# Performance work log

Hardware: AMD Instinct MI355X
Metric: run time of the kernel (lower is better)

## Reference

```python
import jax, jax.numpy as jnp
import numpy as np

B, C, V, L = 64, 32, 1024, 12
C_OUT = 64
ORDER = 2
C_CAT = (ORDER * 3 + 1) * C  # 224


def setup_inputs() -> dict:
    key = jax.random.key(0)
    ks = jax.random.split(key, 6)
    x = jax.random.normal(ks[0], (B, C, V, L), dtype=jnp.float32)
    # random non-negative adjacencies, row-normalized like diffusion supports
    def adj(k):
        a = jax.random.uniform(k, (V, V), dtype=jnp.float32)
        return a / jnp.sum(a, axis=1, keepdims=True)
    a0, a1, a2 = adj(ks[1]), adj(ks[2]), adj(ks[3])
    W = jax.random.normal(ks[4], (C_OUT, C_CAT), dtype=jnp.float32) * 0.05
    b = jax.random.normal(ks[5], (C_OUT,), dtype=jnp.float32) * 0.05
    return {"x": x, "a0": a0, "a1": a1, "a2": a2, "W": W, "b": b}


def reference(x, a0, a1, a2, W, b):
    # diffusion propagation: x[b,c,v,l] @ A[v,w] -> [b,c,w,l]
    def prop(z, A):
        return jnp.einsum('ncvl,vw->ncwl', z, A)

    out = [x]
    for A in (a0, a1, a2):
        x1 = prop(x, A)
        out.append(x1)
        x2 = prop(x1, A)  # order=2
        out.append(x2)
    h = jnp.concatenate(out, axis=1)  # [B, 7*C, V, L]
    # 1x1 conv == channel GEMM; dropout is identity at inference
    return jnp.einsum('ncvl,oc->novl', h, W) + b[None, :, None, None]
```

## Files before the change

### kernel.cpp

```cpp
#include <hip/hip_runtime.h>
#include <hip/hip_bf16.h>


typedef __attribute__((ext_vector_type(4))) float  f32x4;
typedef __attribute__((ext_vector_type(8))) short  s16x8;
typedef __attribute__((ext_vector_type(4))) short  s16x4;

__device__ inline short f2bf(float f) {
    unsigned u = __builtin_bit_cast(unsigned, f);
    unsigned r = (u + 0x7FFFu + ((u >> 16) & 1u)) >> 16;
    return (short)r;
}

__device__ inline f32x4 mfma16(s16x8 a, s16x8 b, f32x4 c) {
    return __builtin_amdgcn_mfma_f32_16x16x32_bf16(a, b, c, 0, 0, 0);
}

__device__ inline void gll16(const void* g, void* l) {
    __builtin_amdgcn_global_load_lds(
        (const __attribute__((address_space(1))) void*)g,
        (__attribute__((address_space(3))) void*)l, 16, 0, 0);
}

#define SB0   __builtin_amdgcn_sched_barrier(0)
#define BARM  asm volatile("s_barrier" ::: "memory")
#define LGKM0 asm volatile("s_waitcnt lgkmcnt(0)" ::: "memory")

__global__ __launch_bounds__(256) void cast_x_v2(const float* __restrict__ x,
                                                 short* __restrict__ Xg) {
    __shared__ short Xl[12 * 1040];
    const int bc = blockIdx.x;
    const int t  = threadIdx.x;
    const int b  = bc >> 5;
    const int c  = bc & 31;
    const float4* src = (const float4*)(x + (size_t)bc * 12288);
#pragma unroll
    for (int k = 0; k < 12; ++k) {
        int f4 = k * 256 + t;
        float4 v = src[f4];
        int f  = f4 * 4;
        int vi = f / 12;
        int li = f - vi * 12;
        float vals[4] = {v.x, v.y, v.z, v.w};
#pragma unroll
        for (int e = 0; e < 4; ++e) {
            Xl[li * 1040 + vi] = f2bf(vals[e]);
            if (++li == 12) { li = 0; ++vi; }
        }
    }
    __syncthreads();
#pragma unroll
    for (int k = 0; k < 6; ++k) {
        int ch = k * 256 + t;
        int l  = ch >> 7;
        int v8 = ch & 127;
        *(s16x8*)(Xg + (size_t)(b * 384 + l * 32 + c) * 1024 + v8 * 8) =
            *(const s16x8*)&Xl[l * 1040 + v8 * 8];
    }
}

__global__ __launch_bounds__(256) void cast_a_v2(const float* __restrict__ a0,
                                                 const float* __restrict__ a1,
                                                 const float* __restrict__ a2,
                                                 short* __restrict__ Btall,
                                                 short* __restrict__ Ab) {
    __shared__ float tbuf[32][33];
    const int z = blockIdx.z;
    const float* A = (z == 0) ? a0 : ((z == 1) ? a1 : a2);
    const int v0 = blockIdx.x * 32;
    const int w0 = blockIdx.y * 32;
    const int tr = threadIdx.x >> 3;
    const int tc = (threadIdx.x & 7) << 2;
    float4 val = *(const float4*)&A[(size_t)(v0 + tr) * 1024 + w0 + tc];
    s16x4 sb;
    sb[0] = f2bf(val.x); sb[1] = f2bf(val.y); sb[2] = f2bf(val.z); sb[3] = f2bf(val.w);
    *(s16x4*)(Ab + (size_t)z * 1048576 + (size_t)(v0 + tr) * 1024 + w0 + tc) = sb;
    tbuf[tr][tc + 0] = val.x; tbuf[tr][tc + 1] = val.y;
    tbuf[tr][tc + 2] = val.z; tbuf[tr][tc + 3] = val.w;
    __syncthreads();
    s16x4 st;
#pragma unroll
    for (int i = 0; i < 4; ++i) st[i] = f2bf(tbuf[tc + i][tr]);
    *(s16x4*)(Btall + (size_t)(2 * z) * 1048576 + (size_t)(w0 + tr) * 1024 + v0 + tc) = st;
}

__global__ __launch_bounds__(256, 2) void gemm_bt(const short* __restrict__ Xb, long xz,
                                                  const short* __restrict__ Btb, long bz,
                                                  short* __restrict__ Cb, long cz,
                                                  int crow) {
    __shared__ __align__(16) short Alds[128 * 32];
    __shared__ __align__(16) short Blds[128 * 32];

    const int tid  = threadIdx.x;
    const int lane = tid & 63;
    const int wid  = tid >> 6;
    const int wm   = wid >> 1;
    const int wn   = wid & 1;
    const int m0   = blockIdx.y * 128;
    const int n0   = blockIdx.x * 128;

    const short* X  = Xb  + (size_t)blockIdx.z * xz;
    const short* Bt = Btb + (size_t)blockIdx.z * bz;
    short*       C  = Cb  + (size_t)blockIdx.z * cz;

    const short* Ag = X  + (size_t)(m0 + wid * 32 + (lane >> 2)) * 1024 + (lane & 3) * 8;
    const short* Bg = Bt + (size_t)(n0 + wid * 32 + (lane >> 2)) * 1024 + (lane & 3) * 8;
    short* la = &Alds[wid * 1024];
    short* lb = &Blds[wid * 1024];

    const int lane15 = lane & 15;
    const int lq     = lane >> 4;
    const int ar     = lane15 * 32 + lq * 8;

    f32x4 acc[4][4] = {};

    for (int k0 = 0; k0 < 1024; k0 += 32) {
        __syncthreads();
        gll16(Ag + k0, la);
        gll16(Ag + k0 + 16 * 1024, la + 512);
        gll16(Bg + k0, lb);
        gll16(Bg + k0 + 16 * 1024, lb + 512);
        __syncthreads();

        s16x8 af[4], bf[4];
#pragma unroll
        for (int i = 0; i < 4; ++i)
            af[i] = *(const s16x8*)&Alds[(wm * 64 + i * 16) * 32 + ar];
#pragma unroll
        for (int j = 0; j < 4; ++j)
            bf[j] = *(const s16x8*)&Blds[(wn * 64 + j * 16) * 32 + ar];
#pragma unroll
        for (int i = 0; i < 4; ++i)
#pragma unroll
            for (int j = 0; j < 4; ++j)
                acc[i][j] = mfma16(af[i], bf[j], acc[i][j]);
    }

#pragma unroll
    for (int i = 0; i < 4; ++i) {
        int rbase = m0 + wm * 64 + i * 16 + lq * 4;
#pragma unroll
        for (int r = 0; r < 4; ++r) {
            size_t rowoff = (size_t)(rbase + r) * crow;
#pragma unroll
            for (int j = 0; j < 4; ++j) {
                int col = n0 + wn * 64 + j * 16 + lane15;
                C[rowoff + col] = f2bf(acc[i][j][r]);
            }
        }
    }
}


#define STAGE_A(d, h, kt) do {                                               \
    const short* _s = Agp + (h) * 65536 + (kt) * 64;                         \
    short* _l = lA + (((d) * 2 + (h)) << 13);                                \
    gll16(_s, _l);                                                           \
    gll16(_s + 131072, _l + 4096);                                           \
} while (0)

#define STAGE_B(d, h, kt) do {                                               \
    const short* _s = Bgp + (h) * 32768 + (kt) * 64;                         \
    short* _l = lB + (((d) * 2 + (h)) << 13);                                \
    gll16(_s, _l);                                                           \
    gll16(_s + 131072, _l + 4096);                                           \
} while (0)

#define RD_A(D, MH) do {                                                     \
    const short* _p = Als + (((D) * 2 + (MH)) << 13) + aBase;                \
    _Pragma("unroll")                                                        \
    for (int _fm = 0; _fm < 4; ++_fm) {                                      \
        af[_fm][0] = *(const s16x8*)(_p + _fm * 1024 + slot0);               \
        af[_fm][1] = *(const s16x8*)(_p + _fm * 1024 + (slot0 ^ 32));        \
    }                                                                        \
} while (0)

#define RD_B(D, NH, dst) do {                                                \
    const short* _p = Bls + (((D) * 2 + (NH)) << 13) + bBase;                \
    _Pragma("unroll")                                                        \
    for (int _fn = 0; _fn < 2; ++_fn) {                                      \
        dst[_fn][0] = *(const s16x8*)(_p + _fn * 1024 + slot0);              \
        dst[_fn][1] = *(const s16x8*)(_p + _fn * 1024 + (slot0 ^ 32));       \
    }                                                                        \
} while (0)

#define MM(MH, NH, bv) do {                                                  \
    __builtin_amdgcn_s_setprio(1);                                           \
    _Pragma("unroll")                                                        \
    for (int _fm = 0; _fm < 4; ++_fm) {                                      \
        _Pragma("unroll")                                                    \
        for (int _fn = 0; _fn < 2; ++_fn) {                                  \
            _Pragma("unroll")                                                \
            for (int _kk = 0; _kk < 2; ++_kk)                                \
                acc[(MH) * 4 + _fm][(NH) * 2 + _fn] =                        \
                    mfma16(af[_fm][_kk], bv[_fn][_kk],                       \
                           acc[(MH) * 4 + _fm][(NH) * 2 + _fn]);             \
        }                                                                    \
    }                                                                        \
    __builtin_amdgcn_s_setprio(0);                                           \
} while (0)

#define VM4 asm volatile("s_waitcnt vmcnt(4)" ::: "memory")
#define VM0 asm volatile("s_waitcnt vmcnt(0)" ::: "memory")

#define TILE(D, T, S1, S2, VMST) do {                                        \
                                                             \
    RD_A(D, 0); RD_B(D, 0, bv0);                                             \
    if (S1) STAGE_A(1 - (D), 1, (T) + 1);                                    \
    SB0; BARM; SB0; LGKM0; SB0;                                              \
    MM(0, 0, bv0);                                                           \
    SB0; BARM; SB0;                                                          \
                                                             \
    RD_B(D, 1, bv1);                                                         \
    if (S1) STAGE_B(1 - (D), 1, (T) + 1);                                    \
    SB0; BARM; SB0; LGKM0; SB0;                                              \
    MM(0, 1, bv1);                                                           \
    SB0; BARM; SB0;                                                          \
                                                             \
    RD_A(D, 1);                                                              \
    if (S2) STAGE_A((D), 0, (T) + 2);                                        \
    SB0; BARM; SB0; LGKM0; SB0;                                              \
    MM(1, 1, bv1);                                                           \
    SB0; BARM; SB0;                                                          \
                                                             \
    if (S2) STAGE_B((D), 0, (T) + 2);                                        \
    SB0; BARM; SB0;                                                          \
    MM(1, 0, bv0);                                                           \
    SB0; VMST; BARM; SB0;                                                    \
} while (0)

__global__ __launch_bounds__(512, 2) void gemm256(const short* __restrict__ X,
                                                  const short* __restrict__ Bt,
                                                  short* __restrict__ C) {
    __shared__ __align__(16) short Als[32768];
    __shared__ __align__(16) short Bls[32768];

    const int t    = threadIdx.x;
    const int lane = t & 63;
    const int w    = t >> 6;
    const int wm   = w >> 2;
    const int wn   = w & 3;
    const int r15  = lane & 15;
    const int q    = lane >> 4;
    const int m0   = blockIdx.y << 8;
    const int n0   = blockIdx.x << 8;

    const int srow = t >> 3;
    const int kc8  = (((t & 7) - srow) & 7) * 8;
    const short* Agp = X + (size_t)(m0 + srow) * 1024 + kc8;
    const int rB0  = ((srow >> 5) << 6) | (srow & 31);
    const short* Bgp = Bt + (size_t)(n0 + rB0) * 1024 + kc8;
    short* lA = Als + t * 8;
    short* lB = Bls + t * 8;

    const int slot0 = ((q + r15) & 7) * 8;
    const int aBase = (wm * 64 + r15) * 64;
    const int bBase = (wn * 32 + r15) * 64;

    f32x4 acc[8][4] = {};
    s16x8 af[4][2], bv0[2][2], bv1[2][2];

    STAGE_A(0, 0, 0); STAGE_A(0, 1, 0); STAGE_B(0, 0, 0); STAGE_B(0, 1, 0);
    STAGE_A(1, 0, 1); STAGE_B(1, 0, 1);
    VM4;
    BARM; SB0;

#pragma unroll 1
    for (int it = 0; it < 7; ++it) {
        const int T = it * 2;
        TILE(0, T,     true, true, VM4);
        TILE(1, T + 1, true, true, VM4);
    }
    TILE(0, 14, true,  false, VM0);
    TILE(1, 15, false, false, (void)0);

    const int s_idx  = n0 >> 10;
    const int v_base = (n0 & 1023) + wn * 64 + r15;
    const int ks0    = s_idx * 32 + q * 4;
#pragma unroll
    for (int fmt = 0; fmt < 8; ++fmt) {
        const int gidx = (m0 >> 5) + wm * 4 + (fmt >> 1);
        const int bb   = gidx / 12;
        const int ll   = gidx - bb * 12;
        const int ks   = ks0 + (fmt & 1) * 16;
        const size_t base = (size_t)bb * 12288 + ll;
#pragma unroll
        for (int fnt = 0; fnt < 4; ++fnt) {
            const int v = v_base + fnt * 16;
            s16x4 sv;
            sv[0] = f2bf(acc[fmt][fnt][0]);
            sv[1] = f2bf(acc[fmt][fnt][1]);
            sv[2] = f2bf(acc[fmt][fnt][2]);
            sv[3] = f2bf(acc[fmt][fnt][3]);
            *(s16x4*)(C + (base + (size_t)v * 12) * 192 + ks) = sv;
        }
    }
}

__global__ __launch_bounds__(256, 2) void gemm_fin(const float* __restrict__ x,
                                                   const short* __restrict__ Hc,
                                                   const float* __restrict__ W,
                                                   const float* __restrict__ bias,
                                                   float* __restrict__ out) {
    __shared__ __align__(16) short Wl[64 * 232];
    __shared__ __align__(16) short Hl[3][8192];

    const int t    = threadIdx.x;
    const int lane = t & 63;
    const int wv   = t >> 6;
    const int r15  = lane & 15;
    const int lq   = lane >> 4;
    const int blk  = blockIdx.x;
    const int b    = blk / 48;
    const int p0   = (blk - b * 48) * 256;
    const size_t R0 = (size_t)b * 12288 + p0;

    {
        const int o  = t >> 2;
        const int c0 = (t & 3) * 56;
        const float* wp = W + o * 224 + c0;
        short* d = &Wl[o * 232 + c0];
#pragma unroll
        for (int i = 0; i < 14; ++i) {
            float4 w4 = *(const float4*)(wp + i * 4);
            s16x4 s;
            s[0] = f2bf(w4.x); s[1] = f2bf(w4.y); s[2] = f2bf(w4.z); s[3] = f2bf(w4.w);
            *(s16x4*)(d + i * 4) = s;
        }
    }
    {
        const int c  = t & 31;
        const int pc = t >> 5;
        const float* xp = x + ((size_t)b * 32 + c) * 12288 + p0 + pc * 32;
        const int kc = c >> 3, ko = c & 7;
#pragma unroll
        for (int j4 = 0; j4 < 8; ++j4) {
            float4 v = *(const float4*)(xp + j4 * 4);
            float vals[4] = {v.x, v.y, v.z, v.w};
#pragma unroll
            for (int e = 0; e < 4; ++e) {
                int row = pc * 32 + j4 * 4 + e;
                Hl[0][row * 32 + (((kc + (row >> 1)) & 3) << 3) + ko] = f2bf(vals[e]);
            }
        }
    }
    const int grow = t >> 2;
    const int slot = t & 3;
#define GLLSTEP(step, buf) do {                                              \
    _Pragma("unroll")                                                        \
    for (int _i = 0; _i < 4; ++_i) {                                         \
        int _row = _i * 64 + grow;                                           \
        int _kc  = (slot - (_row >> 1)) & 3;                                 \
        gll16(Hc + (R0 + _row) * 192 + ((step) - 1) * 32 + _kc * 8,          \
              &Hl[buf][(_i * 256 + t) * 8]);                                 \
    }                                                                        \
} while (0)

    GLLSTEP(1, 1);
    GLLSTEP(2, 2);
    LGKM0;
    BARM; SB0;

    f32x4 acc[4][4] = {};

#define FINSTEP(s, buf) do {                                                 \
    s16x8 af[4], bfr[4];                                                     \
    _Pragma("unroll")                                                        \
    for (int _ot = 0; _ot < 4; ++_ot)                                        \
        af[_ot] = *(const s16x8*)&Wl[(_ot * 16 + r15) * 232 + (s) * 32 + lq * 8]; \
    _Pragma("unroll")                                                        \
    for (int _bt = 0; _bt < 4; ++_bt) {                                      \
        int _row = wv * 64 + _bt * 16 + r15;                                 \
        bfr[_bt] = *(const s16x8*)&Hl[buf][_row * 32 + ((((lq) + (_row >> 1)) & 3) << 3)]; \
    }                                                                        \
    _Pragma("unroll")                                                        \
    for (int _ot = 0; _ot < 4; ++_ot) {                                      \
        _Pragma("unroll")                                                    \
        for (int _bt = 0; _bt < 4; ++_bt)                                    \
            acc[_ot][_bt] = mfma16(af[_ot], bfr[_bt], acc[_ot][_bt]);        \
    }                                                                        \
} while (0)

#define VMW(n) asm volatile("s_waitcnt vmcnt(" #n ")" ::: "memory")

    FINSTEP(0, 0);
    BARM; SB0; GLLSTEP(3, 0);
    VMW(8); BARM; SB0;
    FINSTEP(1, 1);
    BARM; SB0; GLLSTEP(4, 1);
    VMW(8); BARM; SB0;
    FINSTEP(2, 2);
    BARM; SB0; GLLSTEP(5, 2);
    VMW(8); BARM; SB0;
    FINSTEP(3, 0);
    BARM; SB0; GLLSTEP(6, 0);
    VMW(8); BARM; SB0;
    FINSTEP(4, 1);
    BARM; SB0;
    VMW(4); BARM; SB0;
    FINSTEP(5, 2);
    BARM; SB0;
    VMW(0); BARM; SB0;
    FINSTEP(6, 0);

#pragma unroll
    for (int ot = 0; ot < 4; ++ot) {
#pragma unroll
        for (int r = 0; r < 4; ++r) {
            const int o = ot * 16 + lq * 4 + r;
            const float bo = bias[o];
            float* op = out + ((size_t)b * 64 + o) * 12288 + p0;
#pragma unroll
            for (int bt = 0; bt < 4; ++bt)
                op[wv * 64 + bt * 16 + r15] = acc[ot][bt][r] + bo;
        }
    }
}

extern "C" void kernel_launch(void* const* d_in, const int* in_sizes, int n_in,
                              void* d_out, int out_size, void* d_ws, size_t ws_size,
                              hipStream_t stream) {
    const float* x  = (const float*)d_in[0];
    const float* a0 = (const float*)d_in[1];
    const float* a1 = (const float*)d_in[2];
    const float* a2 = (const float*)d_in[3];
    const float* W  = (const float*)d_in[4];
    const float* bs = (const float*)d_in[5];
    float* out = (float*)d_out;

    char* ws = (char*)d_ws;
    short* Xg    = (short*)(ws);
    short* Ab    = (short*)(ws + 50331648L);
    short* Btall = (short*)(ws + 56623104L);
    short* Hcat  = (short*)(ws + 69206016L);

    cast_x_v2<<<2048, 256, 0, stream>>>(x, Xg);
    cast_a_v2<<<dim3(32, 32, 3), 256, 0, stream>>>(a0, a1, a2, Btall, Ab);

    gemm_bt<<<dim3(8, 8, 3), 256, 0, stream>>>(
        Btall, 2097152L, Ab, 1048576L, Btall + 1048576L, 2097152L, 1024);

    gemm256<<<dim3(24, 96), 512, 0, stream>>>(Xg, Btall, Hcat);

    gemm_fin<<<3072, 256, 0, stream>>>(x, Hcat, W, bs, out);
}
```

Measured before the change: 745.8 us.

## Stage gemm256 epilogue through LDS and load final-stage H directly to registers

The big propagation GEMM now writes its bf16 results into shared memory first, then stores them to global memory as coalesced 16-byte rows instead of scattered 8-byte stores. The final 1x1-conv kernel drops its triple-buffered global-to-LDS pipeline. It issues all W, x and H loads up front into registers and feeds the H fragments straight into the MFMAs. This cuts write scatter and per-step barriers, but adds an epilogue barrier and raises register pressure in the final kernel.

```diff
diff --git a/kernel.cpp b/kernel.cpp
--- a/kernel.cpp
+++ b/kernel.cpp
@@ -232,8 +232,9 @@
 __global__ __launch_bounds__(512, 2) void gemm256(const short* __restrict__ X,
                                                   const short* __restrict__ Bt,
                                                   short* __restrict__ C) {
-    __shared__ __align__(16) short Als[32768];
-    __shared__ __align__(16) short Bls[32768];
+    __shared__ __align__(16) short LDSU[65536];
+    short* const Als = LDSU;
+    short* const Bls = LDSU + 32768;
 
     const int t    = threadIdx.x;
     const int lane = t & 63;
@@ -274,26 +275,39 @@
     TILE(0, 14, true,  false, VM0);
     TILE(1, 15, false, false, (void)0);
 
-    const int s_idx  = n0 >> 10;
-    const int v_base = (n0 & 1023) + wn * 64 + r15;
-    const int ks0    = s_idx * 32 + q * 4;
+    short* const E = LDSU;
 #pragma unroll
     for (int fmt = 0; fmt < 8; ++fmt) {
-        const int gidx = (m0 >> 5) + wm * 4 + (fmt >> 1);
-        const int bb   = gidx / 12;
-        const int ll   = gidx - bb * 12;
-        const int ks   = ks0 + (fmt & 1) * 16;
-        const size_t base = (size_t)bb * 12288 + ll;
+        const int gl  = wm * 4 + (fmt >> 1);
+        const int c16 = (fmt & 1) * 2 + (q >> 1);
 #pragma unroll
         for (int fnt = 0; fnt < 4; ++fnt) {
-            const int v = v_base + fnt * 16;
+            const int vl = wn * 64 + fnt * 16 + r15;
             s16x4 sv;
             sv[0] = f2bf(acc[fmt][fnt][0]);
             sv[1] = f2bf(acc[fmt][fnt][1]);
             sv[2] = f2bf(acc[fmt][fnt][2]);
             sv[3] = f2bf(acc[fmt][fnt][3]);
-            *(s16x4*)(C + (base + (size_t)v * 12) * 192 + ks) = sv;
-        }
+            *(s16x4*)&E[gl * 8192 + vl * 32 + (((c16 + vl) & 3) << 3) + ((q & 1) << 2)] = sv;
+        }
+    }
+    __syncthreads();
+    const int s_idx = n0 >> 10;
+    const int vg0   = n0 & 1023;
+    const int g0    = m0 >> 5;
+#pragma unroll
+    for (int i = 0; i < 16; ++i) {
+        const int G   = i * 512 + t;
+        const int row = G >> 2;
+        const int c16 = G & 3;
+        const int gl  = row >> 8;
+        const int vl  = row & 255;
+        const int gg  = g0 + gl;
+        const int bb  = gg / 12;
+        const int ll  = gg - bb * 12;
+        s16x8 val = *(const s16x8*)&E[gl * 8192 + vl * 32 + (((c16 + vl) & 3) << 3)];
+        *(s16x8*)(C + ((size_t)bb * 12288 + (size_t)(vg0 + vl) * 12 + ll) * 192
+                    + s_idx * 32 + c16 * 8) = val;
     }
 }
 
@@ -303,7 +317,7 @@
                                                    const float* __restrict__ bias,
                                                    float* __restrict__ out) {
     __shared__ __align__(16) short Wl[64 * 232];
-    __shared__ __align__(16) short Hl[3][8192];
+    __shared__ __align__(16) short Hl0[8192];
 
     const int t    = threadIdx.x;
     const int lane = t & 63;
@@ -315,101 +329,89 @@
     const int p0   = (blk - b * 48) * 256;
     const size_t R0 = (size_t)b * 12288 + p0;
 
+    const int o  = t >> 2;
+    const int c0 = (t & 3) * 56;
+    const float* wp = W + o * 224 + c0;
+    float4 wbuf[14];
+#pragma unroll
+    for (int i = 0; i < 14; ++i) wbuf[i] = *(const float4*)(wp + i * 4);
+
+    const int xc = t & 31, pc = t >> 5;
+    const float* xp = x + ((size_t)b * 32 + xc) * 12288 + p0 + pc * 32;
+    float4 xbuf[8];
+#pragma unroll
+    for (int j = 0; j < 8; ++j) xbuf[j] = *(const float4*)(xp + j * 4);
+
+    const short* hb = Hc + (R0 + wv * 64 + r15) * 192 + lq * 8;
+    s16x8 bH[6][4];
+#pragma unroll
+    for (int s = 0; s < 6; ++s)
+#pragma unroll
+        for (int bt = 0; bt < 4; ++bt)
+            bH[s][bt] = *(const s16x8*)(hb + (size_t)bt * (16 * 192) + s * 32);
+
     {
-        const int o  = t >> 2;
-        const int c0 = (t & 3) * 56;
-        const float* wp = W + o * 224 + c0;
         short* d = &Wl[o * 232 + c0];
 #pragma unroll
         for (int i = 0; i < 14; ++i) {
-            float4 w4 = *(const float4*)(wp + i * 4);
-            s16x4 s;
-            s[0] = f2bf(w4.x); s[1] = f2bf(w4.y); s[2] = f2bf(w4.z); s[3] = f2bf(w4.w);
-            *(s16x4*)(d + i * 4) = s;
+            s16x4 s4;
+            s4[0] = f2bf(wbuf[i].x); s4[1] = f2bf(wbuf[i].y);
+            s4[2] = f2bf(wbuf[i].z); s4[3] = f2bf(wbuf[i].w);
+            *(s16x4*)(d + i * 4) = s4;
         }
     }
     {
-        const int c  = t & 31;
-        const int pc = t >> 5;
-        const float* xp = x + ((size_t)b * 32 + c) * 12288 + p0 + pc * 32;
-        const int kc = c >> 3, ko = c & 7;
+        const int kc = xc >> 3, ko = xc & 7;
 #pragma unroll
         for (int j4 = 0; j4 < 8; ++j4) {
-            float4 v = *(const float4*)(xp + j4 * 4);
-            float vals[4] = {v.x, v.y, v.z, v.w};
+            float vals[4] = {xbuf[j4].x, xbuf[j4].y, xbuf[j4].z, xbuf[j4].w};
 #pragma unroll
             for (int e = 0; e < 4; ++e) {
                 int row = pc * 32 + j4 * 4 + e;
-                Hl[0][row * 32 + (((kc + (row >> 1)) & 3) << 3) + ko] = f2bf(vals[e]);
+                Hl0[row * 32 + (((kc + (row >> 1)) & 3) << 3) + ko] = f2bf(vals[e]);
             }
         }
     }
-    const int grow = t >> 2;
-    const int slot = t & 3;
-#define GLLSTEP(step, buf) do {                                              \
-    _Pragma("unroll")                                                        \
-    for (int _i = 0; _i < 4; ++_i) {                                         \
-        int _row = _i * 64 + grow;                                           \
-        int _kc  = (slot - (_row >> 1)) & 3;                                 \
-        gll16(Hc + (R0 + _row) * 192 + ((step) - 1) * 32 + _kc * 8,          \
-              &Hl[buf][(_i * 256 + t) * 8]);                                 \
-    }                                                                        \
-} while (0)
-
-    GLLSTEP(1, 1);
-    GLLSTEP(2, 2);
-    LGKM0;
-    BARM; SB0;
+    __syncthreads();
 
     f32x4 acc[4][4] = {};
 
-#define FINSTEP(s, buf) do {                                                 \
-    s16x8 af[4], bfr[4];                                                     \
-    _Pragma("unroll")                                                        \
-    for (int _ot = 0; _ot < 4; ++_ot)                                        \
-        af[_ot] = *(const s16x8*)&Wl[(_ot * 16 + r15) * 232 + (s) * 32 + lq * 8]; \
-    _Pragma("unroll")                                                        \
-    for (int _bt = 0; _bt < 4; ++_bt) {                                      \
-        int _row = wv * 64 + _bt * 16 + r15;                                 \
-        bfr[_bt] = *(const s16x8*)&Hl[buf][_row * 32 + ((((lq) + (_row >> 1)) & 3) << 3)]; \
-    }                                                                        \
-    _Pragma("unroll")                                                        \
-    for (int _ot = 0; _ot < 4; ++_ot) {                                      \
-        _Pragma("unroll")                                                    \
-        for (int _bt = 0; _bt < 4; ++_bt)                                    \
-            acc[_ot][_bt] = mfma16(af[_ot], bfr[_bt], acc[_ot][_bt]);        \
-    }                                                                        \
-} while (0)
-
-#define VMW(n) asm volatile("s_waitcnt vmcnt(" #n ")" ::: "memory")
-
-    FINSTEP(0, 0);
-    BARM; SB0; GLLSTEP(3, 0);
-    VMW(8); BARM; SB0;
-    FINSTEP(1, 1);
-    BARM; SB0; GLLSTEP(4, 1);
-    VMW(8); BARM; SB0;
-    FINSTEP(2, 2);
-    BARM; SB0; GLLSTEP(5, 2);
-    VMW(8); BARM; SB0;
-    FINSTEP(3, 0);
-    BARM; SB0; GLLSTEP(6, 0);
-    VMW(8); BARM; SB0;
-    FINSTEP(4, 1);
-    BARM; SB0;
-    VMW(4); BARM; SB0;
-    FINSTEP(5, 2);
-    BARM; SB0;
-    VMW(0); BARM; SB0;
-    FINSTEP(6, 0);
+    {
+        s16x8 af[4], bfr[4];
+#pragma unroll
+        for (int ot = 0; ot < 4; ++ot)
+            af[ot] = *(const s16x8*)&Wl[(ot * 16 + r15) * 232 + lq * 8];
+#pragma unroll
+        for (int bt = 0; bt < 4; ++bt) {
+            int row = wv * 64 + bt * 16 + r15;
+            bfr[bt] = *(const s16x8*)&Hl0[row * 32 + (((lq + (row >> 1)) & 3) << 3)];
+        }
+#pragma unroll
+        for (int ot = 0; ot < 4; ++ot)
+#pragma unroll
+            for (int bt = 0; bt < 4; ++bt)
+                acc[ot][bt] = mfma16(af[ot], bfr[bt], acc[ot][bt]);
+    }
+#pragma unroll
+    for (int s = 1; s <= 6; ++s) {
+        s16x8 af[4];
+#pragma unroll
+        for (int ot = 0; ot < 4; ++ot)
+            af[ot] = *(const s16x8*)&Wl[(ot * 16 + r15) * 232 + s * 32 + lq * 8];
+#pragma unroll
+        for (int ot = 0; ot < 4; ++ot)
+#pragma unroll
+            for (int bt = 0; bt < 4; ++bt)
+                acc[ot][bt] = mfma16(af[ot], bH[s - 1][bt], acc[ot][bt]);
+    }
 
 #pragma unroll
     for (int ot = 0; ot < 4; ++ot) {
 #pragma unroll
         for (int r = 0; r < 4; ++r) {
-            const int o = ot * 16 + lq * 4 + r;
-            const float bo = bias[o];
-            float* op = out + ((size_t)b * 64 + o) * 12288 + p0;
+            const int oo = ot * 16 + lq * 4 + r;
+            const float bo = bias[oo];
+            float* op = out + ((size_t)b * 64 + oo) * 12288 + p0;
 #pragma unroll
             for (int bt = 0; bt < 4; ++bt)
                 op[wv * 64 + bt * 16 + r15] = acc[ot][bt][r] + bo;
```

Result: faster. 720.2 us (-3.4%).
